# Optimization experiments

Hardware: AMD Instinct MI355X
Metric: run time of the kernel (lower is better)

Reference implementation:

```python
import jax, jax.numpy as jnp
import numpy as np

BH, N, C, T = 16, 2048, 64, 64


def setup_inputs() -> dict:
    key = jax.random.key(0)
    k1, k2, k3 = jax.random.split(key, 3)
    q = jax.random.normal(k1, (BH, N, C), dtype=jnp.float32)
    qk = jax.random.normal(k2, (BH, N, N), dtype=jnp.float32)
    # learned positional embedding (1, C, T); random instead of zeros so the
    # gather/interpolation path is numerically non-trivial
    pos_emb = jax.random.normal(k3, (1, C, T), dtype=jnp.float32)
    return {"q": q, "qk": qk, "pos_emb": pos_emb}


def reference(q, qk, pos_emb):
    T_ = pos_emb.shape[-1]
    # gate: g_ij = sigmoid(q_i . k_j)
    G = jax.nn.sigmoid(qk)                                   # (BH, N, N)
    # reverse cumulative sum along last dim: p_ij = sum_{k=j..N-1} g_ik
    P = jnp.flip(jnp.cumsum(jnp.flip(G, axis=-1), axis=-1), axis=-1)
    P = jnp.minimum(P, T_ - 1)                                # clamp(max=T-1)
    P_ceil = jnp.ceil(P).astype(jnp.int32)                    # (BH, N, N)
    P_floor = jnp.floor(P).astype(jnp.int32)
    # E[b, n, t] = q[b, n, :] @ pos_emb[0, :, t]  -> (BH, N, T)
    E = jnp.einsum('bnc,ct->bnt', q, pos_emb[0])
    E_ceil = jnp.take_along_axis(E, P_ceil, axis=-1)          # (BH, N, N)
    E_floor = jnp.take_along_axis(E, P_floor, axis=-1)
    w = P - P_floor
    return w * E_ceil + (1.0 - w) * E_floor
```

## Files before the change

### kernel.cpp

```cpp
#include <hip/hip_runtime.h>

#define NN    2048
#define CC    64
#define TT    64
#define GRID  2048
#define ITERS 16
#define NROWS (16 * 2048)

__global__ __launch_bounds__(256, 4) void cope_kernel(
    const float* __restrict__ q,
    const float* __restrict__ qk,
    const float* __restrict__ pos_emb,
    float* __restrict__ out)
{
    const int tid  = threadIdx.x;
    const int lane = tid & 63;
    const int wv   = tid >> 6;

    __shared__ float pe[CC * TT];
    __shared__ float wave_tot[2][4];

    {
        const float4* src = (const float4*)pos_emb;
        float4* dst = (float4*)pe;
#pragma unroll
        for (int i = 0; i < (CC * TT / 4) / 256; ++i)
            dst[tid + i * 256] = src[tid + i * 256];
    }

    int row = blockIdx.x;
    const float4* qkp = (const float4*)(qk + (size_t)row * NN);
    float4 a0 = qkp[2 * tid];
    float4 a1 = qkp[2 * tid + 1];

    __syncthreads();

    for (int it = 0; it < ITERS; ++it) {
        float4 b0 = a0, b1 = a1;
        if (it + 1 < ITERS) {
            const float4* np = (const float4*)(qk + (size_t)(row + GRID) * NN);
            b0 = np[2 * tid];
            b1 = np[2 * tid + 1];
        }

        float e;
        {
            const float* qr = q + (size_t)row * CC;
            float acc0 = 0.0f, acc1 = 0.0f;
#pragma unroll 8
            for (int c = 0; c < CC; c += 2) {
                acc0 = fmaf(qr[c],     pe[c * TT + lane],       acc0);
                acc1 = fmaf(qr[c + 1], pe[(c + 1) * TT + lane], acc1);
            }
            e = acc0 + acc1;
        }

        float g[8];
        g[0] = a0.x; g[1] = a0.y; g[2] = a0.z; g[3] = a0.w;
        g[4] = a1.x; g[5] = a1.y; g[6] = a1.z; g[7] = a1.w;
#pragma unroll
        for (int k = 0; k < 8; ++k)
            g[k] = __builtin_amdgcn_rcpf(1.0f + __expf(-g[k]));

        float s = 0.0f;
#pragma unroll
        for (int k = 0; k < 8; ++k) s += g[k];

        float inc = s;
#pragma unroll
        for (int o = 1; o < 64; o <<= 1) {
            float t = __shfl_down(inc, o, 64);
            if (lane + o < 64) inc += t;
        }
        const float X = inc - s;
        if (lane == 0) wave_tot[it & 1][wv] = inc;
        __syncthreads();

        float W = 0.0f;
#pragma unroll
        for (int w2 = 0; w2 < 4; ++w2)
            if (w2 > wv) W += wave_tot[it & 1][w2];
        const float base = X + W;

        float o8[8];
        float run = 0.0f;
#pragma unroll
        for (int k = 7; k >= 0; --k) {
            run += g[k];
            float P  = fminf(run + base, 63.0f);
            float fl = floorf(P);
            float w_ = P - fl;
            int   i0 = (int)fl;
            int   i1 = min(i0 + 1, 63);
            float ef = __shfl(e, i0, 64);
            float ec = __shfl(e, i1, 64);
            o8[k] = fmaf(w_, ec - ef, ef);
        }

        float4* op = (float4*)(out + (size_t)row * NN);
        op[2 * tid]     = make_float4(o8[0], o8[1], o8[2], o8[3]);
        op[2 * tid + 1] = make_float4(o8[4], o8[5], o8[6], o8[7]);

        a0 = b0; a1 = b1;
        row += GRID;
    }
}

extern "C" void kernel_launch(void* const* d_in, const int* in_sizes, int n_in,
                              void* d_out, int out_size, void* d_ws, size_t ws_size,
                              hipStream_t stream) {
    const float* q       = (const float*)d_in[0];
    const float* qk      = (const float*)d_in[1];
    const float* pos_emb = (const float*)d_in[2];
    float* out = (float*)d_out;

    dim3 grid(GRID);
    dim3 block(256);
    cope_kernel<<<grid, block, 0, stream>>>(q, qk, pos_emb, out);
}
```

Baseline: 124.4 us.

## Map one row per wavefront and drop LDS, barriers and row loop

```diff
diff --git a/kernel.cpp b/kernel.cpp
--- a/kernel.cpp
+++ b/kernel.cpp
@@ -1,13 +1,10 @@
 #include <hip/hip_runtime.h>
 
-#define NN    2048
-#define CC    64
-#define TT    64
-#define GRID  2048
-#define ITERS 16
-#define NROWS (16 * 2048)
+#define NN 2048
+#define CC 64
+#define TT 64
 
-__global__ __launch_bounds__(256, 4) void cope_kernel(
+__global__ __launch_bounds__(256, 8) void cope_kernel(
     const float* __restrict__ q,
     const float* __restrict__ qk,
     const float* __restrict__ pos_emb,
@@ -16,93 +13,62 @@
     const int tid  = threadIdx.x;
     const int lane = tid & 63;
     const int wv   = tid >> 6;
+    const int row  = (blockIdx.x << 2) | wv;
+    const int urow = __builtin_amdgcn_readfirstlane(row);
 
-    __shared__ float pe[CC * TT];
-    __shared__ float wave_tot[2][4];
+    const float4* qk4 = (const float4*)(qk + (size_t)row * NN);
+    float4 v[8];
+#pragma unroll
+    for (int i = 0; i < 8; ++i) v[i] = qk4[lane * 8 + i];
 
-    {
-        const float4* src = (const float4*)pos_emb;
-        float4* dst = (float4*)pe;
+    const float* qr = q + (size_t)urow * CC;
+    float acc0 = 0.0f, acc1 = 0.0f;
+#pragma unroll 4
+    for (int c = 0; c < CC; c += 2) {
+        acc0 = fmaf(qr[c],     pos_emb[c * TT + lane],       acc0);
+        acc1 = fmaf(qr[c + 1], pos_emb[(c + 1) * TT + lane], acc1);
+    }
+    const float e_lo = acc0 + acc1;
+    const float e_hi = __shfl(e_lo, min(lane + 1, 63), 64);
+
+    float g[32];
 #pragma unroll
-        for (int i = 0; i < (CC * TT / 4) / 256; ++i)
-            dst[tid + i * 256] = src[tid + i * 256];
+    for (int i = 0; i < 8; ++i) {
+        g[4 * i + 0] = v[i].x; g[4 * i + 1] = v[i].y;
+        g[4 * i + 2] = v[i].z; g[4 * i + 3] = v[i].w;
+    }
+    float s = 0.0f;
+#pragma unroll
+    for (int k = 0; k < 32; ++k) {
+        g[k] = __builtin_amdgcn_rcpf(1.0f + __expf(-g[k]));
+        s += g[k];
     }
 
-    int row = blockIdx.x;
-    const float4* qkp = (const float4*)(qk + (size_t)row * NN);
-    float4 a0 = qkp[2 * tid];
-    float4 a1 = qkp[2 * tid + 1];
+    float inc = s;
+#pragma unroll
+    for (int o = 1; o < 64; o <<= 1) {
+        float t = __shfl_down(inc, o, 64);
+        if (lane + o < 64) inc += t;
+    }
+    const float X = inc - s;
 
-    __syncthreads();
-
-    for (int it = 0; it < ITERS; ++it) {
-        float4 b0 = a0, b1 = a1;
-        if (it + 1 < ITERS) {
-            const float4* np = (const float4*)(qk + (size_t)(row + GRID) * NN);
-            b0 = np[2 * tid];
-            b1 = np[2 * tid + 1];
+    float4* op = (float4*)(out + (size_t)row * NN);
+    float run = 0.0f;
+#pragma unroll
+    for (int i = 7; i >= 0; --i) {
+        float o4[4];
+#pragma unroll
+        for (int c = 3; c >= 0; --c) {
+            run += g[4 * i + c];
+            float P  = fminf(run + X, 63.0f);
+            float fl = floorf(P);
+            float w  = P - fl;
+            int   i0 = (int)fl;
+            float ef = __shfl(e_lo, i0, 64);
+            float ec = __shfl(e_hi, i0, 64);
+            o4[c] = fmaf(w, ec - ef, ef);
         }
-
-        float e;
-        {
-            const float* qr = q + (size_t)row * CC;
-            float acc0 = 0.0f, acc1 = 0.0f;
-#pragma unroll 8
-            for (int c = 0; c < CC; c += 2) {
-                acc0 = fmaf(qr[c],     pe[c * TT + lane],       acc0);
-                acc1 = fmaf(qr[c + 1], pe[(c + 1) * TT + lane], acc1);
-            }
-            e = acc0 + acc1;
-        }
-
-        float g[8];
-        g[0] = a0.x; g[1] = a0.y; g[2] = a0.z; g[3] = a0.w;
-        g[4] = a1.x; g[5] = a1.y; g[6] = a1.z; g[7] = a1.w;
-#pragma unroll
-        for (int k = 0; k < 8; ++k)
-            g[k] = __builtin_amdgcn_rcpf(1.0f + __expf(-g[k]));
-
-        float s = 0.0f;
-#pragma unroll
-        for (int k = 0; k < 8; ++k) s += g[k];
-
-        float inc = s;
-#pragma unroll
-        for (int o = 1; o < 64; o <<= 1) {
-            float t = __shfl_down(inc, o, 64);
-            if (lane + o < 64) inc += t;
-        }
-        const float X = inc - s;
-        if (lane == 0) wave_tot[it & 1][wv] = inc;
-        __syncthreads();
-
-        float W = 0.0f;
-#pragma unroll
-        for (int w2 = 0; w2 < 4; ++w2)
-            if (w2 > wv) W += wave_tot[it & 1][w2];
-        const float base = X + W;
-
-        float o8[8];
-        float run = 0.0f;
-#pragma unroll
-        for (int k = 7; k >= 0; --k) {
-            run += g[k];
-            float P  = fminf(run + base, 63.0f);
-            float fl = floorf(P);
-            float w_ = P - fl;
-            int   i0 = (int)fl;
-            int   i1 = min(i0 + 1, 63);
-            float ef = __shfl(e, i0, 64);
-            float ec = __shfl(e, i1, 64);
-            o8[k] = fmaf(w_, ec - ef, ef);
-        }
-
-        float4* op = (float4*)(out + (size_t)row * NN);
-        op[2 * tid]     = make_float4(o8[0], o8[1], o8[2], o8[3]);
-        op[2 * tid + 1] = make_float4(o8[4], o8[5], o8[6], o8[7]);
-
-        a0 = b0; a1 = b1;
-        row += GRID;
+        op[lane * 8 + i] = make_float4(o4[0], o4[1], o4[2], o4[3]);
     }
 }
 
@@ -114,7 +80,7 @@
     const float* pos_emb = (const float*)d_in[2];
     float* out = (float*)d_out;
 
-    dim3 grid(GRID);
+    dim3 grid((16 * 2048) / 4);
     dim3 block(256);
     cope_kernel<<<grid, block, 0, stream>>>(q, qk, pos_emb, out);
 }
```

Result: slower. 158.2 us (+27.2%).
